# Kernel optimization log

Measured on AMD Instinct MI355X. Metric: run time of the kernel, lower is better.

The kernel has to match this reference:

```python
import jax, jax.numpy as jnp
import numpy as np

B, S, N, D, H, C = 64, 4, 4096, 1024, 16, 14
HD = D // H
EPS = 1e-5


def _ln(x, g, b):
    m = jnp.mean(x, axis=-1, keepdims=True)
    v = jnp.mean((x - m) ** 2, axis=-1, keepdims=True)
    return (x - m) * jax.lax.rsqrt(v + EPS) * g + b


def setup_inputs() -> dict:
    key = jax.random.key(0)
    ks = jax.random.split(key, 12)
    std = 0.02
    return {
        "cls_tok": jax.random.normal(ks[0], (B, D), jnp.float32),
        "storage": jax.random.normal(ks[1], (B, S, D), jnp.float32),
        "patches": jax.random.normal(ks[2], (B, N, D), jnp.float32),
        "query": jax.random.normal(ks[3], (1, 1, D), jnp.float32) * std,
        "ln_kv_g": jnp.ones((D,), jnp.float32),
        "ln_kv_b": jnp.zeros((D,), jnp.float32),
        "Wq": jax.random.normal(ks[4], (D, D), jnp.float32) / np.sqrt(D).astype(np.float32),
        "Wk": jax.random.normal(ks[5], (D, D), jnp.float32) / np.sqrt(D).astype(np.float32),
        "Wv": jax.random.normal(ks[6], (D, D), jnp.float32) / np.sqrt(D).astype(np.float32),
        "bq": jnp.zeros((D,), jnp.float32),
        "bk": jnp.zeros((D,), jnp.float32),
        "bv": jnp.zeros((D,), jnp.float32),
        "Wo": jax.random.normal(ks[7], (D, D), jnp.float32) / np.sqrt(D).astype(np.float32),
        "bo": jnp.zeros((D,), jnp.float32),
        "ln_out_g": jnp.ones((D,), jnp.float32),
        "ln_out_b": jnp.zeros((D,), jnp.float32),
        "Wp": jax.random.normal(ks[8], (C, D), jnp.float32) * std,
        "bp": jnp.zeros((C,), jnp.float32),
    }


def reference(cls_tok, storage, patches, query, ln_kv_g, ln_kv_b,
              Wq, Wk, Wv, bq, bk, bv, Wo, bo, ln_out_g, ln_out_b, Wp, bp):
    # tokens: (B, L, D) with L = 1 + S + N
    tokens = jnp.concatenate([cls_tok[:, None, :], storage, patches], axis=1)
    kv = _ln(tokens, ln_kv_g, ln_kv_b)
    b = tokens.shape[0]
    q = jnp.broadcast_to(query, (b, 1, D))
    # torch MultiheadAttention: separate q/k/v projections then scaled dot-product
    qp = (q @ Wq.T + bq).reshape(b, 1, H, HD)
    kp = (kv @ Wk.T + bk).reshape(b, -1, H, HD)
    vp = (kv @ Wv.T + bv).reshape(b, -1, H, HD)
    scale = 1.0 / np.sqrt(HD).astype(np.float32)
    scores = jnp.einsum('bqhd,bkhd->bhqk', qp, kp) * scale  # (B, H, 1, L)
    attn = jax.nn.softmax(scores, axis=-1)
    ctx = jnp.einsum('bhqk,bkhd->bqhd', attn, vp).reshape(b, 1, D)
    pooled = ctx[:, 0] @ Wo.T + bo          # out projection, (B, D)
    pooled = _ln(pooled, ln_out_g, ln_out_b)
    return pooled @ Wp.T + bp               # (B, num_labels)
```

## Files before the change

kernel.cpp:

```cpp
#include <hip/hip_runtime.h>
#include <hip/hip_bf16.h>

#define BB 64
#define DD 1024
#define HH 16
#define LL 4101
#define NCH 8
#define CHUNK 513
#define SCALE 0.125f
#define LN_EPS 1e-5f

typedef float  f32x4 __attribute__((ext_vector_type(4)));
typedef short  s16x8 __attribute__((ext_vector_type(8)));
typedef unsigned int u32x4 __attribute__((ext_vector_type(4)));

#define WS_QVEC 0
#define WS_GU   1024
#define WS_G    17408
#define WS_BU   17424
#define WS_CB   17440
#define WS_PL   17456
#define WS_PM   25648
#define WS_PA   33840
#define WS_CTX  8422448
#define WS_POOL 8487984

__device__ __forceinline__ unsigned int pk2(float a, float b) {
    __hip_bfloat162 h = __float22bfloat162_rn(make_float2(a, b));
    unsigned int r;
    __builtin_memcpy(&r, &h, 4);
    return r;
}

__global__ void k_qvec(const float* __restrict__ query, const float* __restrict__ Wq,
                       const float* __restrict__ bq, float* __restrict__ qvec) {
    int j = blockIdx.x; int lane = threadIdx.x;
    const float4* wr = reinterpret_cast<const float4*>(Wq + (size_t)j * DD);
    const float4* qr = reinterpret_cast<const float4*>(query);
    float s = 0.f;
#pragma unroll
    for (int k = 0; k < 4; ++k) {
        float4 a = wr[k * 64 + lane];
        float4 q = qr[k * 64 + lane];
        s += a.x * q.x + a.y * q.y + a.z * q.z + a.w * q.w;
    }
#pragma unroll
    for (int m = 1; m < 64; m <<= 1) s += __shfl_xor(s, m, 64);
    if (lane == 0) qvec[j] = s + bq[j];
}

__global__ void k_u(const float* __restrict__ Wk, const float* __restrict__ qvec,
                    const float* __restrict__ g, const float* __restrict__ bln,
                    float* __restrict__ gu, float* __restrict__ Gv, float* __restrict__ Bu) {
    int h = blockIdx.x; int tid = threadIdx.x;
    int w = tid >> 6, lane = tid & 63;
    __shared__ float qs[64];
    __shared__ float red[8];
    if (tid < 64) qs[tid] = qvec[h * 64 + tid];
    __syncthreads();
    int d0 = tid * 4;
    float ax = 0.f, ay = 0.f, az = 0.f, aw = 0.f;
    for (int i = 0; i < 64; ++i) {
        float q = qs[i];
        float4 wv = *reinterpret_cast<const float4*>(&Wk[(size_t)(h * 64 + i) * DD + d0]);
        ax += q * wv.x; ay += q * wv.y; az += q * wv.z; aw += q * wv.w;
    }
    float4 g4 = *reinterpret_cast<const float4*>(&g[d0]);
    float4 b4 = *reinterpret_cast<const float4*>(&bln[d0]);
    float ux = ax * SCALE, uy = ay * SCALE, uz = az * SCALE, uw = aw * SCALE;
    float4 gu4 = make_float4(ux * g4.x, uy * g4.y, uz * g4.z, uw * g4.w);
    *reinterpret_cast<float4*>(&gu[(size_t)h * DD + d0]) = gu4;
    float Gp = gu4.x + gu4.y + gu4.z + gu4.w;
    float Bp = ux * b4.x + uy * b4.y + uz * b4.z + uw * b4.w;
#pragma unroll
    for (int m = 1; m < 64; m <<= 1) { Gp += __shfl_xor(Gp, m, 64); Bp += __shfl_xor(Bp, m, 64); }
    if (lane == 0) { red[2 * w] = Gp; red[2 * w + 1] = Bp; }
    __syncthreads();
    if (tid == 0) {
        Gv[h] = red[0] + red[2] + red[4] + red[6];
        Bu[h] = red[1] + red[3] + red[5] + red[7];
    }
}

__global__ void k_cq(const float* __restrict__ qvec, const float* __restrict__ bk,
                     const float* __restrict__ Bu, float* __restrict__ CB) {
    int h = threadIdx.x;
    if (h < HH) {
        float s = 0.f;
        for (int i = 0; i < 64; ++i) s += qvec[h * 64 + i] * bk[h * 64 + i];
        CB[h] = Bu[h] + s * SCALE;
    }
}

__global__ __launch_bounds__(256, 2) void k_main(
    const float* __restrict__ cls, const float* __restrict__ sto,
    const float* __restrict__ pat, const float* __restrict__ gu,
    const float* __restrict__ Gv, const float* __restrict__ CBv,
    float* __restrict__ pA, float* __restrict__ pl, float* __restrict__ pM) {

    __shared__ __align__(16) ushort Xlds[32 * 1024];
    __shared__ __align__(16) f32x4 csr[4][2][64];
    __shared__ __align__(16) ushort alds[512];
    __shared__ float2 mrs[32];

    const int blk = blockIdx.x;
    const int b = blk >> 3, ch = blk & 7;
    const int row0 = ch * CHUNK;
    const int rows = min(CHUNK, LL - row0);
    const int nt = (rows + 31) >> 5;
    const int tid = threadIdx.x;
    const int w = tid >> 6, lane = tid & 63;
    const int lm = lane & 15, lg = lane >> 4;

    s16x8 guf[8];
    {
        const float* gubase = gu + (size_t)lm * DD + w * 256 + lg * 8;
#pragma unroll
        for (int s = 0; s < 8; ++s) {
            const float* p = gubase + s * 32;
            u32x4 t;
#pragma unroll
            for (int j = 0; j < 4; ++j) t[j] = pk2(p[2 * j], p[2 * j + 1]);
            guf[s] = __builtin_bit_cast(s16x8, t);
        }
    }
    const float Gh = Gv[lm], CBh = CBv[lm];

    f32x4 acc[16];
#pragma unroll
    for (int i = 0; i < 16; ++i) acc[i] = (f32x4){0.f, 0.f, 0.f, 0.f};
    float lacc = 0.f, macc = 0.f;

    const int C0 = (lm >> 2) * 4096 + w * 1024 + (lg >> 1) * 64 + (lm & 3) * 16 + (lg & 1) * 8;
    const int bbase = lg * 8192 + w * 1024 + lm;
    const int aoff = lm * 32 + lg * 8;

    for (int t = 0; t < nt; ++t) {
#pragma unroll 2
        for (int rr = 0; rr < 8; ++rr) {
            int rl = w * 8 + rr;
            int rloc = t * 32 + rl;
            bool valid = rloc < rows;
            float4 v[4];
            if (valid) {
                int gr = row0 + rloc;
                const float* src;
                if (gr == 0)      src = cls + (size_t)b * DD;
                else if (gr <= 4) src = sto + ((size_t)b * 4 + (gr - 1)) * DD;
                else              src = pat + ((size_t)b * 4096 + (gr - 5)) * DD;
                const float4* s4 = reinterpret_cast<const float4*>(src);
#pragma unroll
                for (int it = 0; it < 4; ++it) v[it] = s4[it * 64 + lane];
            } else {
#pragma unroll
                for (int it = 0; it < 4; ++it) v[it] = make_float4(0.f, 0.f, 0.f, 0.f);
            }
            float s1 = 0.f, s2 = 0.f;
#pragma unroll
            for (int it = 0; it < 4; ++it) {
                float4 q = v[it];
                s1 += q.x + q.y + q.z + q.w;
                s2 += q.x * q.x + q.y * q.y + q.z * q.z + q.w * q.w;
                uint2 pk;
                pk.x = pk2(q.x, q.y);
                pk.y = pk2(q.z, q.w);
                int d0 = 4 * (it * 64 + lane);
                int elem = ((rl >> 2) * 64 + (d0 >> 4)) * 64 + ((rl & 3) << 4) + (d0 & 15);
                *reinterpret_cast<uint2*>(&Xlds[elem]) = pk;
            }
#pragma unroll
            for (int m = 1; m < 64; m <<= 1) {
                s1 += __shfl_xor(s1, m, 64);
                s2 += __shfl_xor(s2, m, 64);
            }
            if (lane == 0) {
                float mean = s1 * (1.f / 1024.f);
                float var = s2 * (1.f / 1024.f) - mean * mean;
                float rstd = rsqrtf(var + LN_EPS);
                mrs[rl] = make_float2(rstd, -mean * rstd);
            }
        }
        __syncthreads();

        {
            f32x4 c0 = {0.f, 0.f, 0.f, 0.f}, c1 = {0.f, 0.f, 0.f, 0.f};
#pragma unroll
            for (int s = 0; s < 8; ++s) {
                s16x8 a0 = *reinterpret_cast<const s16x8*>(&Xlds[C0 + s * 128]);
                s16x8 a1 = *reinterpret_cast<const s16x8*>(&Xlds[C0 + 16384 + s * 128]);
                c0 = __builtin_amdgcn_mfma_f32_16x16x32_bf16(a0, guf[s], c0, 0, 0, 0);
                c1 = __builtin_amdgcn_mfma_f32_16x16x32_bf16(a1, guf[s], c1, 0, 0, 0);
            }
            csr[w][0][lane] = c0;
            csr[w][1][lane] = c1;
        }
        __syncthreads();

        if (w == 0) {
            f32x4 d0v = csr[0][0][lane], d1v = csr[0][1][lane];
#pragma unroll
            for (int wp = 1; wp < 4; ++wp) {
                f32x4 e0 = csr[wp][0][lane], e1 = csr[wp][1][lane];
                d0v += e0; d1v += e1;
            }
#pragma unroll
            for (int tt = 0; tt < 2; ++tt) {
                f32x4 dv = tt ? d1v : d0v;
                int rbase = tt * 16 + lg * 4;
                float al[4];
#pragma unroll
                for (int i = 0; i < 4; ++i) {
                    float2 mr = mrs[rbase + i];
                    float sc = dv[i] * mr.x + (mr.y * Gh + CBh);
                    bool vld = (t * 32 + rbase + i) < rows;
                    float p = vld ? __expf(sc) : 0.f;
                    lacc += p;
                    macc += p * mr.y;
                    al[i] = p * mr.x;
                }
                unsigned int q0 = pk2(al[0], al[1]);
                unsigned int q1 = pk2(al[2], al[3]);
                *reinterpret_cast<unsigned int*>(&alds[lm * 32 + rbase])     = q0;
                *reinterpret_cast<unsigned int*>(&alds[lm * 32 + rbase + 2]) = q1;
            }
        }
        __syncthreads();

        {
            s16x8 af = *reinterpret_cast<const s16x8*>(&alds[aoff]);
#pragma unroll
            for (int dt = 0; dt < 16; ++dt) {
                s16x8 bfrag;
#pragma unroll
                for (int j = 0; j < 8; ++j) {
                    int e = bbase + dt * 64 + ((j & 3) << 4) + ((j >> 2) << 12);
                    bfrag[j] = (short)Xlds[e];
                }
                acc[dt] = __builtin_amdgcn_mfma_f32_16x16x32_bf16(af, bfrag, acc[dt], 0, 0, 0);
            }
        }
        __syncthreads();
    }

    size_t pabase = ((size_t)blk << 14);
#pragma unroll
    for (int dt = 0; dt < 16; ++dt) {
#pragma unroll
        for (int i = 0; i < 4; ++i) {
            int h = lg * 4 + i;
            pA[pabase + ((size_t)h << 10) + w * 256 + dt * 16 + lm] = acc[dt][i];
        }
    }
    if (w == 0) {
        lacc += __shfl_xor(lacc, 16, 64); lacc += __shfl_xor(lacc, 32, 64);
        macc += __shfl_xor(macc, 16, 64); macc += __shfl_xor(macc, 32, 64);
        if (lane < 16) {
            pl[blk * 16 + lane] = lacc;
            pM[blk * 16 + lane] = -macc;
        }
    }
}

__global__ void k_comb(float* __restrict__ pA, const float* __restrict__ pl,
                       const float* __restrict__ pM, const float* __restrict__ g,
                       const float* __restrict__ bln) {
    int blk = blockIdx.x; int b = blk >> 4; int h = blk & 15; int tid = threadIdx.x;
    float l = 0.f, M = 0.f;
#pragma unroll
    for (int ch = 0; ch < NCH; ++ch) {
        l += pl[(b * NCH + ch) * 16 + h];
        M += pM[(b * NCH + ch) * 16 + h];
    }
    float inv = 1.f / l;
    float4 s = make_float4(0.f, 0.f, 0.f, 0.f);
#pragma unroll
    for (int ch = 0; ch < NCH; ++ch) {
        const float4* p4 = reinterpret_cast<const float4*>(
            pA + (((size_t)(b * NCH + ch) * 16 + h) << 10));
        float4 v = p4[tid];
        s.x += v.x; s.y += v.y; s.z += v.z; s.w += v.w;
    }
    float4 g4 = *reinterpret_cast<const float4*>(&g[tid * 4]);
    float4 b4 = *reinterpret_cast<const float4*>(&bln[tid * 4]);
    float4 o;
    o.x = g4.x * (s.x - M) * inv + b4.x;
    o.y = g4.y * (s.y - M) * inv + b4.y;
    o.z = g4.z * (s.z - M) * inv + b4.z;
    o.w = g4.w * (s.w - M) * inv + b4.w;
    float4* dst = reinterpret_cast<float4*>(pA + (((size_t)(b * NCH) * 16 + h) << 10));
    dst[tid] = o;
}

__global__ void k_ctx(const float* __restrict__ Wv, const float* __restrict__ bv,
                      const float* __restrict__ pA, float* __restrict__ ctx) {
    int j = blockIdx.x; int h = j >> 6;
    int w = threadIdx.x >> 6, lane = threadIdx.x & 63;
    const float4* wr = reinterpret_cast<const float4*>(Wv + (size_t)j * DD);
    float4 wv[4];
#pragma unroll
    for (int k = 0; k < 4; ++k) wv[k] = wr[k * 64 + lane];
    float bvj = bv[j];
    for (int bb2 = w * 16; bb2 < w * 16 + 16; ++bb2) {
        const float4* sr = reinterpret_cast<const float4*>(
            pA + (((size_t)(bb2 * NCH) * 16 + h) << 10));
        float s = 0.f;
#pragma unroll
        for (int k = 0; k < 4; ++k) {
            float4 v = sr[k * 64 + lane];
            s += wv[k].x * v.x + wv[k].y * v.y + wv[k].z * v.z + wv[k].w * v.w;
        }
#pragma unroll
        for (int m = 1; m < 64; m <<= 1) s += __shfl_xor(s, m, 64);
        if (lane == 0) ctx[(size_t)bb2 * DD + j] = s + bvj;
    }
}

__global__ void k_pool(const float* __restrict__ Wo, const float* __restrict__ bo,
                       const float* __restrict__ ctx, float* __restrict__ pooled) {
    int j = blockIdx.x;
    int w = threadIdx.x >> 6, lane = threadIdx.x & 63;
    const float4* wr = reinterpret_cast<const float4*>(Wo + (size_t)j * DD);
    float4 wv[4];
#pragma unroll
    for (int k = 0; k < 4; ++k) wv[k] = wr[k * 64 + lane];
    float boj = bo[j];
    for (int bb2 = w * 16; bb2 < w * 16 + 16; ++bb2) {
        const float4* cr4 = reinterpret_cast<const float4*>(ctx + (size_t)bb2 * DD);
        float s = 0.f;
#pragma unroll
        for (int k = 0; k < 4; ++k) {
            float4 v = cr4[k * 64 + lane];
            s += wv[k].x * v.x + wv[k].y * v.y + wv[k].z * v.z + wv[k].w * v.w;
        }
#pragma unroll
        for (int m = 1; m < 64; m <<= 1) s += __shfl_xor(s, m, 64);
        if (lane == 0) pooled[(size_t)bb2 * DD + j] = s + boj;
    }
}

__global__ void k_head(const float* __restrict__ pooled, const float* __restrict__ g2,
                       const float* __restrict__ b2, const float* __restrict__ Wp,
                       const float* __restrict__ bp, float* __restrict__ out) {
    int b = blockIdx.x; int tid = threadIdx.x;
    __shared__ float pln[DD];
    __shared__ float red[8];
    const float4* pr = reinterpret_cast<const float4*>(pooled + (size_t)b * DD);
    float4 v = pr[tid];
    float s1 = v.x + v.y + v.z + v.w;
    float s2 = v.x * v.x + v.y * v.y + v.z * v.z + v.w * v.w;
#pragma unroll
    for (int m = 1; m < 64; m <<= 1) { s1 += __shfl_xor(s1, m, 64); s2 += __shfl_xor(s2, m, 64); }
    int w = tid >> 6, lane = tid & 63;
    if (lane == 0) { red[2 * w] = s1; red[2 * w + 1] = s2; }
    __syncthreads();
    s1 = red[0] + red[2] + red[4] + red[6];
    s2 = red[1] + red[3] + red[5] + red[7];
    float mean = s1 * (1.f / 1024.f);
    float var  = s2 * (1.f / 1024.f) - mean * mean;
    float rstd = rsqrtf(var + LN_EPS);
    int d0 = tid * 4;
    pln[d0 + 0] = (v.x - mean) * rstd * g2[d0 + 0] + b2[d0 + 0];
    pln[d0 + 1] = (v.y - mean) * rstd * g2[d0 + 1] + b2[d0 + 1];
    pln[d0 + 2] = (v.z - mean) * rstd * g2[d0 + 2] + b2[d0 + 2];
    pln[d0 + 3] = (v.w - mean) * rstd * g2[d0 + 3] + b2[d0 + 3];
    __syncthreads();
    int q = tid & 15, c = tid >> 4;
    if (c < 14) {
        float s = 0.f;
#pragma unroll 8
        for (int i = 0; i < 64; ++i) {
            int d = i * 16 + q;
            s += pln[d] * Wp[c * DD + d];
        }
#pragma unroll
        for (int m = 1; m < 16; m <<= 1) s += __shfl_xor(s, m, 64);
        if (q == 0) out[b * 14 + c] = s + bp[c];
    }
}

extern "C" void kernel_launch(void* const* d_in, const int* in_sizes, int n_in,
                              void* d_out, int out_size, void* d_ws, size_t ws_size,
                              hipStream_t stream) {
    const float* cls   = (const float*)d_in[0];
    const float* sto   = (const float*)d_in[1];
    const float* pat   = (const float*)d_in[2];
    const float* query = (const float*)d_in[3];
    const float* g     = (const float*)d_in[4];
    const float* bln   = (const float*)d_in[5];
    const float* Wq    = (const float*)d_in[6];
    const float* Wk    = (const float*)d_in[7];
    const float* Wv    = (const float*)d_in[8];
    const float* bq    = (const float*)d_in[9];
    const float* bk    = (const float*)d_in[10];
    const float* bv    = (const float*)d_in[11];
    const float* Wo    = (const float*)d_in[12];
    const float* bo    = (const float*)d_in[13];
    const float* g2    = (const float*)d_in[14];
    const float* b2    = (const float*)d_in[15];
    const float* Wp    = (const float*)d_in[16];
    const float* bp    = (const float*)d_in[17];

    float* ws     = (float*)d_ws;
    float* qvec   = ws + WS_QVEC;
    float* gu     = ws + WS_GU;
    float* Gv     = ws + WS_G;
    float* Bu     = ws + WS_BU;
    float* CB     = ws + WS_CB;
    float* pl     = ws + WS_PL;
    float* pM     = ws + WS_PM;
    float* pA     = ws + WS_PA;
    float* ctx    = ws + WS_CTX;
    float* pooled = ws + WS_POOL;
    float* out    = (float*)d_out;

    hipLaunchKernelGGL(k_qvec, dim3(1024), dim3(64), 0, stream, query, Wq, bq, qvec);
    hipLaunchKernelGGL(k_u,    dim3(16),   dim3(256), 0, stream, Wk, qvec, g, bln, gu, Gv, Bu);
    hipLaunchKernelGGL(k_cq,   dim3(1),    dim3(64), 0, stream, qvec, bk, Bu, CB);
    hipLaunchKernelGGL(k_main, dim3(BB * NCH), dim3(256), 0, stream,
                       cls, sto, pat, gu, Gv, CB, pA, pl, pM);
    hipLaunchKernelGGL(k_comb, dim3(BB * HH), dim3(256), 0, stream, pA, pl, pM, g, bln);
    hipLaunchKernelGGL(k_ctx,  dim3(1024), dim3(256), 0, stream, Wv, bv, pA, ctx);
    hipLaunchKernelGGL(k_pool, dim3(1024), dim3(256), 0, stream, Wo, bo, ctx, pooled);
    hipLaunchKernelGGL(k_head, dim3(64),   dim3(256), 0, stream, pooled, g2, b2, Wp, bp, out);
}
```

Before: 279.2 us.

## Prefetch next tile rows into registers and compute LayerNorm stats with MFMA

Half of each wave's rows for the next 32-row tile are now loaded into registers while the current tile is being computed. They are converted to bf16 and written to LDS at the start of the next iteration, so global memory latency overlaps with the MFMA work. The per-row mean and sum-of-squares shuffle reductions are replaced by extra MFMAs (X·X and X·ones) on the bf16 LDS tile. All waves now redundantly compute the softmax weights, which removes a barrier, and the remaining __syncthreads calls become raw s_barrier calls. The LDS row-group stride is padded to 4104 to reduce bank conflicts. In exchange, register pressure goes up and the LayerNorm statistics are computed from bf16-rounded values, which costs some accuracy.

```diff
diff --git a/kernel.cpp b/kernel.cpp
--- a/kernel.cpp
+++ b/kernel.cpp
@@ -9,6 +9,7 @@
 #define CHUNK 513
 #define SCALE 0.125f
 #define LN_EPS 1e-5f
+#define RGS 4104
 
 typedef float  f32x4 __attribute__((ext_vector_type(4)));
 typedef short  s16x8 __attribute__((ext_vector_type(8)));
@@ -30,6 +31,30 @@
     unsigned int r;
     __builtin_memcpy(&r, &h, 4);
     return r;
+}
+
+__device__ __forceinline__ const float* rowptr(int gr, int b, const float* cls,
+                                               const float* sto, const float* pat) {
+    if (gr == 0) return cls + (size_t)b * DD;
+    if (gr <= 4) return sto + ((size_t)b * 4 + (gr - 1)) * DD;
+    return pat + ((size_t)b * 4096 + (gr - 5)) * DD;
+}
+
+__device__ __forceinline__ void pfload(float4 (&pf)[4][4], int tt, int nt, int rows, int row0,
+                                       int b, int w, int lane,
+                                       const float* cls, const float* sto, const float* pat) {
+#pragma unroll
+    for (int rr = 0; rr < 4; ++rr) {
+#pragma unroll
+        for (int it = 0; it < 4; ++it) pf[rr][it] = make_float4(0.f, 0.f, 0.f, 0.f);
+        int rloc = tt * 32 + w * 8 + rr;
+        if (tt < nt && rloc < rows) {
+            const float4* s4 = reinterpret_cast<const float4*>(
+                rowptr(row0 + rloc, b, cls, sto, pat));
+#pragma unroll
+            for (int it = 0; it < 4; ++it) pf[rr][it] = s4[it * 64 + lane];
+        }
+    }
 }
 
 __global__ void k_qvec(const float* __restrict__ query, const float* __restrict__ Wq,
@@ -98,8 +123,9 @@
     const float* __restrict__ Gv, const float* __restrict__ CBv,
     float* __restrict__ pA, float* __restrict__ pl, float* __restrict__ pM) {
 
-    __shared__ __align__(16) ushort Xlds[32 * 1024];
+    __shared__ __align__(16) ushort Xlds[8 * RGS];
     __shared__ __align__(16) f32x4 csr[4][2][64];
+    __shared__ float sstat[4][2][32];
     __shared__ __align__(16) ushort alds[512];
     __shared__ float2 mrs[32];
 
@@ -124,6 +150,10 @@
             guf[s] = __builtin_bit_cast(s16x8, t);
         }
     }
+    s16x8 ones;
+#pragma unroll
+    for (int j = 0; j < 8; ++j) ones[j] = (short)0x3F80;
+
     const float Gh = Gv[lm], CBh = CBv[lm];
 
     f32x4 acc[16];
@@ -131,77 +161,112 @@
     for (int i = 0; i < 16; ++i) acc[i] = (f32x4){0.f, 0.f, 0.f, 0.f};
     float lacc = 0.f, macc = 0.f;
 
-    const int C0 = (lm >> 2) * 4096 + w * 1024 + (lg >> 1) * 64 + (lm & 3) * 16 + (lg & 1) * 8;
-    const int bbase = lg * 8192 + w * 1024 + lm;
+    const int C0   = (lm >> 2) * RGS + w * 1024 + (lg >> 1) * 64 + (lm & 3) * 16 + (lg & 1) * 8;
+    const int A1O  = 4 * RGS;
+    const int bb4  = lg * 2 * RGS + w * 1024 + lm;
     const int aoff = lm * 32 + lg * 8;
 
+    float4 pf[4][4];
+    uint2  nx[4][4];
+
+    pfload(pf, 0, nt, rows, row0, b, w, lane, cls, sto, pat);
+#pragma unroll
+    for (int rr = 0; rr < 4; ++rr)
+#pragma unroll
+        for (int it = 0; it < 4; ++it) {
+            nx[rr][it].x = pk2(pf[rr][it].x, pf[rr][it].y);
+            nx[rr][it].y = pk2(pf[rr][it].z, pf[rr][it].w);
+        }
+
     for (int t = 0; t < nt; ++t) {
+#pragma unroll
+        for (int rr = 0; rr < 4; ++rr) {
+            int rl = w * 8 + rr;
+#pragma unroll
+            for (int it = 0; it < 4; ++it) {
+                int d0 = 4 * (it * 64 + lane);
+                int elem = (rl >> 2) * RGS + (d0 >> 4) * 64 + (rl & 3) * 16 + (d0 & 15);
+                *reinterpret_cast<uint2*>(&Xlds[elem]) = nx[rr][it];
+            }
+        }
 #pragma unroll 2
-        for (int rr = 0; rr < 8; ++rr) {
+        for (int rr = 4; rr < 8; ++rr) {
             int rl = w * 8 + rr;
             int rloc = t * 32 + rl;
             bool valid = rloc < rows;
             float4 v[4];
+#pragma unroll
+            for (int it = 0; it < 4; ++it) v[it] = make_float4(0.f, 0.f, 0.f, 0.f);
             if (valid) {
-                int gr = row0 + rloc;
-                const float* src;
-                if (gr == 0)      src = cls + (size_t)b * DD;
-                else if (gr <= 4) src = sto + ((size_t)b * 4 + (gr - 1)) * DD;
-                else              src = pat + ((size_t)b * 4096 + (gr - 5)) * DD;
-                const float4* s4 = reinterpret_cast<const float4*>(src);
+                const float4* s4 = reinterpret_cast<const float4*>(
+                    rowptr(row0 + rloc, b, cls, sto, pat));
 #pragma unroll
                 for (int it = 0; it < 4; ++it) v[it] = s4[it * 64 + lane];
-            } else {
-#pragma unroll
-                for (int it = 0; it < 4; ++it) v[it] = make_float4(0.f, 0.f, 0.f, 0.f);
-            }
-            float s1 = 0.f, s2 = 0.f;
+            }
 #pragma unroll
             for (int it = 0; it < 4; ++it) {
-                float4 q = v[it];
-                s1 += q.x + q.y + q.z + q.w;
-                s2 += q.x * q.x + q.y * q.y + q.z * q.z + q.w * q.w;
                 uint2 pk;
-                pk.x = pk2(q.x, q.y);
-                pk.y = pk2(q.z, q.w);
+                pk.x = pk2(v[it].x, v[it].y);
+                pk.y = pk2(v[it].z, v[it].w);
                 int d0 = 4 * (it * 64 + lane);
-                int elem = ((rl >> 2) * 64 + (d0 >> 4)) * 64 + ((rl & 3) << 4) + (d0 & 15);
+                int elem = (rl >> 2) * RGS + (d0 >> 4) * 64 + (rl & 3) * 16 + (d0 & 15);
                 *reinterpret_cast<uint2*>(&Xlds[elem]) = pk;
             }
-#pragma unroll
-            for (int m = 1; m < 64; m <<= 1) {
-                s1 += __shfl_xor(s1, m, 64);
-                s2 += __shfl_xor(s2, m, 64);
-            }
-            if (lane == 0) {
-                float mean = s1 * (1.f / 1024.f);
-                float var = s2 * (1.f / 1024.f) - mean * mean;
-                float rstd = rsqrtf(var + LN_EPS);
-                mrs[rl] = make_float2(rstd, -mean * rstd);
-            }
-        }
-        __syncthreads();
+        }
+        pfload(pf, t + 1, nt, rows, row0, b, w, lane, cls, sto, pat);
+
+        asm volatile("s_waitcnt lgkmcnt(0)" ::: "memory");
+        __builtin_amdgcn_s_barrier();
 
         {
-            f32x4 c0 = {0.f, 0.f, 0.f, 0.f}, c1 = {0.f, 0.f, 0.f, 0.f};
+            f32x4 c0 = {0.f,0.f,0.f,0.f}, c1 = {0.f,0.f,0.f,0.f};
+            f32x4 q0 = {0.f,0.f,0.f,0.f}, q1 = {0.f,0.f,0.f,0.f};
+            f32x4 m0 = {0.f,0.f,0.f,0.f}, m1 = {0.f,0.f,0.f,0.f};
 #pragma unroll
             for (int s = 0; s < 8; ++s) {
                 s16x8 a0 = *reinterpret_cast<const s16x8*>(&Xlds[C0 + s * 128]);
-                s16x8 a1 = *reinterpret_cast<const s16x8*>(&Xlds[C0 + 16384 + s * 128]);
+                s16x8 a1 = *reinterpret_cast<const s16x8*>(&Xlds[C0 + A1O + s * 128]);
                 c0 = __builtin_amdgcn_mfma_f32_16x16x32_bf16(a0, guf[s], c0, 0, 0, 0);
                 c1 = __builtin_amdgcn_mfma_f32_16x16x32_bf16(a1, guf[s], c1, 0, 0, 0);
+                q0 = __builtin_amdgcn_mfma_f32_16x16x32_bf16(a0, a0,     q0, 0, 0, 0);
+                q1 = __builtin_amdgcn_mfma_f32_16x16x32_bf16(a1, a1,     q1, 0, 0, 0);
+                m0 = __builtin_amdgcn_mfma_f32_16x16x32_bf16(a0, ones,   m0, 0, 0, 0);
+                m1 = __builtin_amdgcn_mfma_f32_16x16x32_bf16(a1, ones,   m1, 0, 0, 0);
             }
             csr[w][0][lane] = c0;
             csr[w][1][lane] = c1;
-        }
-        __syncthreads();
-
-        if (w == 0) {
+            if (lg == (lm >> 2)) {
+                sstat[w][0][lm]      = q0[lm & 3];
+                sstat[w][0][16 + lm] = q1[lm & 3];
+            }
+            if (lm == 0) {
+#pragma unroll
+                for (int i = 0; i < 4; ++i) {
+                    sstat[w][1][lg * 4 + i]      = m0[i];
+                    sstat[w][1][16 + lg * 4 + i] = m1[i];
+                }
+            }
+        }
+        asm volatile("s_waitcnt lgkmcnt(0)" ::: "memory");
+        __builtin_amdgcn_s_barrier();
+
+        if (lane < 32) {
+            int r = lane;
+            float s2 = sstat[0][0][r] + sstat[1][0][r] + sstat[2][0][r] + sstat[3][0][r];
+            float s1 = sstat[0][1][r] + sstat[1][1][r] + sstat[2][1][r] + sstat[3][1][r];
+            float mean = s1 * (1.f / 1024.f);
+            float var  = s2 * (1.f / 1024.f) - mean * mean;
+            float rstd = rsqrtf(var + LN_EPS);
+            mrs[r] = make_float2(rstd, -mean * rstd);
+        }
+        asm volatile("s_waitcnt lgkmcnt(0)" ::: "memory");
+        __builtin_amdgcn_sched_barrier(0);
+        {
             f32x4 d0v = csr[0][0][lane], d1v = csr[0][1][lane];
 #pragma unroll
             for (int wp = 1; wp < 4; ++wp) {
-                f32x4 e0 = csr[wp][0][lane], e1 = csr[wp][1][lane];
-                d0v += e0; d1v += e1;
+                d0v += csr[wp][0][lane];
+                d1v += csr[wp][1][lane];
             }
 #pragma unroll
             for (int tt = 0; tt < 2; ++tt) {
@@ -218,13 +283,20 @@
                     macc += p * mr.y;
                     al[i] = p * mr.x;
                 }
-                unsigned int q0 = pk2(al[0], al[1]);
-                unsigned int q1 = pk2(al[2], al[3]);
-                *reinterpret_cast<unsigned int*>(&alds[lm * 32 + rbase])     = q0;
-                *reinterpret_cast<unsigned int*>(&alds[lm * 32 + rbase + 2]) = q1;
-            }
-        }
-        __syncthreads();
+                *reinterpret_cast<unsigned int*>(&alds[lm * 32 + rbase])     = pk2(al[0], al[1]);
+                *reinterpret_cast<unsigned int*>(&alds[lm * 32 + rbase + 2]) = pk2(al[2], al[3]);
+            }
+        }
+        asm volatile("s_waitcnt lgkmcnt(0)" ::: "memory");
+        __builtin_amdgcn_sched_barrier(0);
+
+#pragma unroll
+        for (int rr = 0; rr < 4; ++rr)
+#pragma unroll
+            for (int it = 0; it < 4; ++it) {
+                nx[rr][it].x = pk2(pf[rr][it].x, pf[rr][it].y);
+                nx[rr][it].y = pk2(pf[rr][it].z, pf[rr][it].w);
+            }
 
         {
             s16x8 af = *reinterpret_cast<const s16x8*>(&alds[aoff]);
@@ -233,13 +305,14 @@
                 s16x8 bfrag;
 #pragma unroll
                 for (int j = 0; j < 8; ++j) {
-                    int e = bbase + dt * 64 + ((j & 3) << 4) + ((j >> 2) << 12);
+                    int e = bb4 + dt * 64 + ((j & 3) << 4) + (j >> 2) * RGS;
                     bfrag[j] = (short)Xlds[e];
                 }
                 acc[dt] = __builtin_amdgcn_mfma_f32_16x16x32_bf16(af, bfrag, acc[dt], 0, 0, 0);
             }
         }
-        __syncthreads();
+        asm volatile("s_waitcnt lgkmcnt(0)" ::: "memory");
+        __builtin_amdgcn_s_barrier();
     }
 
     size_t pabase = ((size_t)blk << 14);
```

After: 370.8 us. +32.8%, slower.

## Double k_main block to 512 threads and pad LDS row-group stride

Applied to the files above, without the earlier changes.

The streaming attention kernel now runs 8 waves per block instead of 4. Each wave loads half as many rows per tile, the score MFMA is split across two wave groups, and each wave holds half as many output accumulators. Every wave now computes the softmax weights redundantly, which removes one block-wide barrier in favour of a local LDS wait. The LDS row-group stride is padded to 4104 elements to reduce bank conflicts. The aim is more memory-level parallelism while streaming the large patch tensor. The costs are tighter per-thread register limits from launch_bounds(512,4), possible spilling, and an LDS footprint that caps how many blocks fit per CU.

```diff
diff --git a/kernel.cpp b/kernel.cpp
--- a/kernel.cpp
+++ b/kernel.cpp
@@ -9,6 +9,7 @@
 #define CHUNK 513
 #define SCALE 0.125f
 #define LN_EPS 1e-5f
+#define RGS 4104
 
 typedef float  f32x4 __attribute__((ext_vector_type(4)));
 typedef short  s16x8 __attribute__((ext_vector_type(8)));
@@ -30,6 +31,13 @@
     unsigned int r;
     __builtin_memcpy(&r, &h, 4);
     return r;
+}
+
+__device__ __forceinline__ const float* rowptr(int gr, int b, const float* cls,
+                                               const float* sto, const float* pat) {
+    if (gr == 0) return cls + (size_t)b * DD;
+    if (gr <= 4) return sto + ((size_t)b * 4 + (gr - 1)) * DD;
+    return pat + ((size_t)b * 4096 + (gr - 5)) * DD;
 }
 
 __global__ void k_qvec(const float* __restrict__ query, const float* __restrict__ Wq,
@@ -92,14 +100,14 @@
     }
 }
 
-__global__ __launch_bounds__(256, 2) void k_main(
+__global__ __launch_bounds__(512, 4) void k_main(
     const float* __restrict__ cls, const float* __restrict__ sto,
     const float* __restrict__ pat, const float* __restrict__ gu,
     const float* __restrict__ Gv, const float* __restrict__ CBv,
     float* __restrict__ pA, float* __restrict__ pl, float* __restrict__ pM) {
 
-    __shared__ __align__(16) ushort Xlds[32 * 1024];
-    __shared__ __align__(16) f32x4 csr[4][2][64];
+    __shared__ __align__(16) ushort Xlds[8 * RGS];
+    __shared__ __align__(16) f32x4 csr[8][64];
     __shared__ __align__(16) ushort alds[512];
     __shared__ float2 mrs[32];
 
@@ -111,10 +119,11 @@
     const int tid = threadIdx.x;
     const int w = tid >> 6, lane = tid & 63;
     const int lm = lane & 15, lg = lane >> 4;
+    const int g = w >> 2, wk = w & 3;
 
     s16x8 guf[8];
     {
-        const float* gubase = gu + (size_t)lm * DD + w * 256 + lg * 8;
+        const float* gubase = gu + (size_t)lm * DD + wk * 256 + lg * 8;
 #pragma unroll
         for (int s = 0; s < 8; ++s) {
             const float* p = gubase + s * 32;
@@ -126,34 +135,29 @@
     }
     const float Gh = Gv[lm], CBh = CBv[lm];
 
-    f32x4 acc[16];
-#pragma unroll
-    for (int i = 0; i < 16; ++i) acc[i] = (f32x4){0.f, 0.f, 0.f, 0.f};
+    f32x4 acc[8];
+#pragma unroll
+    for (int i = 0; i < 8; ++i) acc[i] = (f32x4){0.f, 0.f, 0.f, 0.f};
     float lacc = 0.f, macc = 0.f;
 
-    const int C0 = (lm >> 2) * 4096 + w * 1024 + (lg >> 1) * 64 + (lm & 3) * 16 + (lg & 1) * 8;
-    const int bbase = lg * 8192 + w * 1024 + lm;
+    const int C0   = (g * 4 + (lm >> 2)) * RGS + wk * 1024 + (lg >> 1) * 64 + (lm & 3) * 16 + (lg & 1) * 8;
+    const int bb4  = lg * 2 * RGS + w * 512 + lm;
     const int aoff = lm * 32 + lg * 8;
 
     for (int t = 0; t < nt; ++t) {
-#pragma unroll 2
-        for (int rr = 0; rr < 8; ++rr) {
-            int rl = w * 8 + rr;
+#pragma unroll
+        for (int rr = 0; rr < 4; ++rr) {
+            int rl = w * 4 + rr;
             int rloc = t * 32 + rl;
             bool valid = rloc < rows;
             float4 v[4];
+#pragma unroll
+            for (int it = 0; it < 4; ++it) v[it] = make_float4(0.f, 0.f, 0.f, 0.f);
             if (valid) {
-                int gr = row0 + rloc;
-                const float* src;
-                if (gr == 0)      src = cls + (size_t)b * DD;
-                else if (gr <= 4) src = sto + ((size_t)b * 4 + (gr - 1)) * DD;
-                else              src = pat + ((size_t)b * 4096 + (gr - 5)) * DD;
-                const float4* s4 = reinterpret_cast<const float4*>(src);
+                const float4* s4 = reinterpret_cast<const float4*>(
+                    rowptr(row0 + rloc, b, cls, sto, pat));
 #pragma unroll
                 for (int it = 0; it < 4; ++it) v[it] = s4[it * 64 + lane];
-            } else {
-#pragma unroll
-                for (int it = 0; it < 4; ++it) v[it] = make_float4(0.f, 0.f, 0.f, 0.f);
             }
             float s1 = 0.f, s2 = 0.f;
 #pragma unroll
@@ -165,7 +169,7 @@
                 pk.x = pk2(q.x, q.y);
                 pk.y = pk2(q.z, q.w);
                 int d0 = 4 * (it * 64 + lane);
-                int elem = ((rl >> 2) * 64 + (d0 >> 4)) * 64 + ((rl & 3) << 4) + (d0 & 15);
+                int elem = (rl >> 2) * RGS + (d0 >> 4) * 64 + (rl & 3) * 16 + (d0 & 15);
                 *reinterpret_cast<uint2*>(&Xlds[elem]) = pk;
             }
 #pragma unroll
@@ -183,30 +187,23 @@
         __syncthreads();
 
         {
-            f32x4 c0 = {0.f, 0.f, 0.f, 0.f}, c1 = {0.f, 0.f, 0.f, 0.f};
+            f32x4 c0 = {0.f, 0.f, 0.f, 0.f};
 #pragma unroll
             for (int s = 0; s < 8; ++s) {
                 s16x8 a0 = *reinterpret_cast<const s16x8*>(&Xlds[C0 + s * 128]);
-                s16x8 a1 = *reinterpret_cast<const s16x8*>(&Xlds[C0 + 16384 + s * 128]);
                 c0 = __builtin_amdgcn_mfma_f32_16x16x32_bf16(a0, guf[s], c0, 0, 0, 0);
-                c1 = __builtin_amdgcn_mfma_f32_16x16x32_bf16(a1, guf[s], c1, 0, 0, 0);
-            }
-            csr[w][0][lane] = c0;
-            csr[w][1][lane] = c1;
+            }
+            csr[w][lane] = c0;
         }
         __syncthreads();
 
-        if (w == 0) {
-            f32x4 d0v = csr[0][0][lane], d1v = csr[0][1][lane];
-#pragma unroll
-            for (int wp = 1; wp < 4; ++wp) {
-                f32x4 e0 = csr[wp][0][lane], e1 = csr[wp][1][lane];
-                d0v += e0; d1v += e1;
-            }
-#pragma unroll
-            for (int tt = 0; tt < 2; ++tt) {
-                f32x4 dv = tt ? d1v : d0v;
-                int rbase = tt * 16 + lg * 4;
+        {
+#pragma unroll
+            for (int gg = 0; gg < 2; ++gg) {
+                f32x4 dv = csr[gg * 4][lane];
+#pragma unroll
+                for (int wp = 1; wp < 4; ++wp) dv += csr[gg * 4 + wp][lane];
+                int rbase = gg * 16 + lg * 4;
                 float al[4];
 #pragma unroll
                 for (int i = 0; i < 4; ++i) {
@@ -218,22 +215,21 @@
                     macc += p * mr.y;
                     al[i] = p * mr.x;
                 }
-                unsigned int q0 = pk2(al[0], al[1]);
-                unsigned int q1 = pk2(al[2], al[3]);
-                *reinterpret_cast<unsigned int*>(&alds[lm * 32 + rbase])     = q0;
-                *reinterpret_cast<unsigned int*>(&alds[lm * 32 + rbase + 2]) = q1;
-            }
-        }
-        __syncthreads();
+                *reinterpret_cast<unsigned int*>(&alds[lm * 32 + rbase])     = pk2(al[0], al[1]);
+                *reinterpret_cast<unsigned int*>(&alds[lm * 32 + rbase + 2]) = pk2(al[2], al[3]);
+            }
+        }
+        asm volatile("s_waitcnt lgkmcnt(0)" ::: "memory");
+        __builtin_amdgcn_sched_barrier(0);
 
         {
             s16x8 af = *reinterpret_cast<const s16x8*>(&alds[aoff]);
 #pragma unroll
-            for (int dt = 0; dt < 16; ++dt) {
+            for (int dt = 0; dt < 8; ++dt) {
                 s16x8 bfrag;
 #pragma unroll
                 for (int j = 0; j < 8; ++j) {
-                    int e = bbase + dt * 64 + ((j & 3) << 4) + ((j >> 2) << 12);
+                    int e = bb4 + dt * 64 + ((j & 3) << 4) + (j >> 2) * RGS;
                     bfrag[j] = (short)Xlds[e];
                 }
                 acc[dt] = __builtin_amdgcn_mfma_f32_16x16x32_bf16(af, bfrag, acc[dt], 0, 0, 0);
@@ -244,11 +240,11 @@
 
     size_t pabase = ((size_t)blk << 14);
 #pragma unroll
-    for (int dt = 0; dt < 16; ++dt) {
+    for (int dt = 0; dt < 8; ++dt) {
 #pragma unroll
         for (int i = 0; i < 4; ++i) {
             int h = lg * 4 + i;
-            pA[pabase + ((size_t)h << 10) + w * 256 + dt * 16 + lm] = acc[dt][i];
+            pA[pabase + ((size_t)h << 10) + w * 128 + dt * 16 + lm] = acc[dt][i];
         }
     }
     if (w == 0) {
@@ -416,7 +412,7 @@
     hipLaunchKernelGGL(k_qvec, dim3(1024), dim3(64), 0, stream, query, Wq, bq, qvec);
     hipLaunchKernelGGL(k_u,    dim3(16),   dim3(256), 0, stream, Wk, qvec, g, bln, gu, Gv, Bu);
     hipLaunchKernelGGL(k_cq,   dim3(1),    dim3(64), 0, stream, qvec, bk, Bu, CB);
-    hipLaunchKernelGGL(k_main, dim3(BB * NCH), dim3(256), 0, stream,
+    hipLaunchKernelGGL(k_main, dim3(BB * NCH), dim3(512), 0, stream,
                        cls, sto, pat, gu, Gv, CB, pA, pl, pM);
     hipLaunchKernelGGL(k_comb, dim3(BB * HH), dim3(256), 0, stream, pA, pl, pM, g, bln);
     hipLaunchKernelGGL(k_ctx,  dim3(1024), dim3(256), 0, stream, Wv, bv, pA, ctx);
```

New measurement: 287.3 us. 1.03x slower.

## Compute LayerNorm row statistics with MFMA instead of wave shuffles

Applied to the files above, without the earlier changes.

Drops the per-row fp32 sum and sum-of-squares shuffle reductions during the load phase. Row sums now come from an MFMA of the bf16 tile against a ones vector, and sums of squares from an MFMA of the tile with itself (diagonal entries kept), both reduced across waves through a small shared buffer. The goal is to take VALU and cross-lane shuffle work off the memory-bound load loop, at the cost of four extra MFMAs per step and statistics computed from bf16-rounded values, which loses precision in the variance.

```diff
diff --git a/kernel.cpp b/kernel.cpp
--- a/kernel.cpp
+++ b/kernel.cpp
@@ -100,6 +100,7 @@
 
     __shared__ __align__(16) ushort Xlds[32 * 1024];
     __shared__ __align__(16) f32x4 csr[4][2][64];
+    __shared__ __align__(16) float sstat[2][32][4];
     __shared__ __align__(16) ushort alds[512];
     __shared__ float2 mrs[32];
 
@@ -121,9 +122,14 @@
             u32x4 t;
 #pragma unroll
             for (int j = 0; j < 4; ++j) t[j] = pk2(p[2 * j], p[2 * j + 1]);
-            guf[s] = __builtin_bit_cast(s16x8, t);
-        }
-    }
+            s16x8 f; __builtin_memcpy(&f, &t, 16);
+            guf[s] = f;
+        }
+    }
+    s16x8 ones;
+#pragma unroll
+    for (int j = 0; j < 8; ++j) ones[j] = (short)0x3F80;
+
     const float Gh = Gv[lm], CBh = CBv[lm];
 
     f32x4 acc[16];
@@ -155,48 +161,62 @@
 #pragma unroll
                 for (int it = 0; it < 4; ++it) v[it] = make_float4(0.f, 0.f, 0.f, 0.f);
             }
-            float s1 = 0.f, s2 = 0.f;
 #pragma unroll
             for (int it = 0; it < 4; ++it) {
-                float4 q = v[it];
-                s1 += q.x + q.y + q.z + q.w;
-                s2 += q.x * q.x + q.y * q.y + q.z * q.z + q.w * q.w;
                 uint2 pk;
-                pk.x = pk2(q.x, q.y);
-                pk.y = pk2(q.z, q.w);
+                pk.x = pk2(v[it].x, v[it].y);
+                pk.y = pk2(v[it].z, v[it].w);
                 int d0 = 4 * (it * 64 + lane);
                 int elem = ((rl >> 2) * 64 + (d0 >> 4)) * 64 + ((rl & 3) << 4) + (d0 & 15);
                 *reinterpret_cast<uint2*>(&Xlds[elem]) = pk;
             }
-#pragma unroll
-            for (int m = 1; m < 64; m <<= 1) {
-                s1 += __shfl_xor(s1, m, 64);
-                s2 += __shfl_xor(s2, m, 64);
-            }
-            if (lane == 0) {
-                float mean = s1 * (1.f / 1024.f);
-                float var = s2 * (1.f / 1024.f) - mean * mean;
-                float rstd = rsqrtf(var + LN_EPS);
-                mrs[rl] = make_float2(rstd, -mean * rstd);
-            }
         }
         __syncthreads();
 
         {
-            f32x4 c0 = {0.f, 0.f, 0.f, 0.f}, c1 = {0.f, 0.f, 0.f, 0.f};
+            f32x4 c0 = {0.f,0.f,0.f,0.f}, c1 = {0.f,0.f,0.f,0.f};
+            f32x4 q0 = {0.f,0.f,0.f,0.f}, q1 = {0.f,0.f,0.f,0.f};
+            f32x4 m0 = {0.f,0.f,0.f,0.f}, m1 = {0.f,0.f,0.f,0.f};
 #pragma unroll
             for (int s = 0; s < 8; ++s) {
                 s16x8 a0 = *reinterpret_cast<const s16x8*>(&Xlds[C0 + s * 128]);
                 s16x8 a1 = *reinterpret_cast<const s16x8*>(&Xlds[C0 + 16384 + s * 128]);
                 c0 = __builtin_amdgcn_mfma_f32_16x16x32_bf16(a0, guf[s], c0, 0, 0, 0);
                 c1 = __builtin_amdgcn_mfma_f32_16x16x32_bf16(a1, guf[s], c1, 0, 0, 0);
+                q0 = __builtin_amdgcn_mfma_f32_16x16x32_bf16(a0, a0,     q0, 0, 0, 0);
+                q1 = __builtin_amdgcn_mfma_f32_16x16x32_bf16(a1, a1,     q1, 0, 0, 0);
+                m0 = __builtin_amdgcn_mfma_f32_16x16x32_bf16(a0, ones,   m0, 0, 0, 0);
+                m1 = __builtin_amdgcn_mfma_f32_16x16x32_bf16(a1, ones,   m1, 0, 0, 0);
             }
             csr[w][0][lane] = c0;
             csr[w][1][lane] = c1;
+            if (lg == (lm >> 2)) {
+                sstat[0][lm][w]      = q0[lm & 3];
+                sstat[0][16 + lm][w] = q1[lm & 3];
+            }
+            if (lm == 0) {
+#pragma unroll
+                for (int i = 0; i < 4; ++i) {
+                    sstat[1][lg * 4 + i][w]      = m0[i];
+                    sstat[1][16 + lg * 4 + i][w] = m1[i];
+                }
+            }
         }
         __syncthreads();
 
         if (w == 0) {
+            if (lane < 32) {
+                f32x4 qv = *reinterpret_cast<const f32x4*>(&sstat[0][lane][0]);
+                f32x4 mv = *reinterpret_cast<const f32x4*>(&sstat[1][lane][0]);
+                float s2 = qv[0] + qv[1] + qv[2] + qv[3];
+                float s1 = mv[0] + mv[1] + mv[2] + mv[3];
+                float mean = s1 * (1.f / 1024.f);
+                float var  = s2 * (1.f / 1024.f) - mean * mean;
+                float rstd = rsqrtf(var + LN_EPS);
+                mrs[lane] = make_float2(rstd, -mean * rstd);
+            }
+            asm volatile("s_waitcnt lgkmcnt(0)" ::: "memory");
+            __builtin_amdgcn_sched_barrier(0);
             f32x4 d0v = csr[0][0][lane], d1v = csr[0][1][lane];
 #pragma unroll
             for (int wp = 1; wp < 4; ++wp) {
@@ -218,10 +238,10 @@
                     macc += p * mr.y;
                     al[i] = p * mr.x;
                 }
-                unsigned int q0 = pk2(al[0], al[1]);
-                unsigned int q1 = pk2(al[2], al[3]);
-                *reinterpret_cast<unsigned int*>(&alds[lm * 32 + rbase])     = q0;
-                *reinterpret_cast<unsigned int*>(&alds[lm * 32 + rbase + 2]) = q1;
+                unsigned int qq0 = pk2(al[0], al[1]);
+                unsigned int qq1 = pk2(al[2], al[3]);
+                *reinterpret_cast<unsigned int*>(&alds[lm * 32 + rbase])     = qq0;
+                *reinterpret_cast<unsigned int*>(&alds[lm * 32 + rbase + 2]) = qq1;
             }
         }
         __syncthreads();
```

Result: faster. 255.1 us (-8.6%).
